# Optimization experiments

Measured on AMD Instinct MI355X. Metric: run time of the kernel, lower is better.

Reference implementation:

```python
import jax, jax.numpy as jnp
import numpy as np

N, L, E, H, D = 4, 2048, 1024, 16, 64

def setup_inputs() -> dict:
    key = jax.random.key(0)
    ks = jax.random.split(key, 8)
    s = 1.0 / np.sqrt(E)
    return {
        "Q": jax.random.normal(ks[0], (N, L, E), jnp.float32),
        "K": jax.random.normal(ks[1], (N, L, E), jnp.float32),
        "V": jax.random.normal(ks[2], (N, L, E), jnp.float32),
        "Wq": jax.random.normal(ks[3], (H * D, E), jnp.float32) * s,
        "bq": jnp.zeros((H * D,), jnp.float32),
        "Wk": jax.random.normal(ks[4], (H * D, E), jnp.float32) * s,
        "bk": jnp.zeros((H * D,), jnp.float32),
        "Wv": jax.random.normal(ks[5], (H * D, E), jnp.float32) * s,
        "bv": jnp.zeros((H * D,), jnp.float32),
        "Wo": jax.random.normal(ks[6], (E, H * D), jnp.float32) * s,
        "bo": jnp.zeros((E,), jnp.float32),
    }

def reference(Q, K, V, Wq, bq, Wk, bk, Wv, bv, Wo, bo):
    n, lq, e = Q.shape
    lk = K.shape[1]
    # projections: Linear(x) = x @ W.T + b
    q = (Q @ Wq.T + bq).reshape(n, lq, H, D)
    k = (K @ Wk.T + bk).reshape(n, lk, H, D)
    v = (V @ Wv.T + bv).reshape(n, lk, H, D)
    # scores over key dim (original broadcasts Q*K and sums over d)
    scores = jnp.einsum('nqhd,nkhd->nqkh', q, k) / jnp.sqrt(jnp.float32(D))
    attn = jax.nn.softmax(scores, axis=2)  # softmax over key axis
    out = jnp.einsum('nqkh,nkhd->nqhd', attn, v)
    out = out.reshape(n, lq, H * D)
    return (out @ Wo.T + bo).reshape(n, lq, E)
```

## Files before the change

kernel.cpp:

```cpp
#include <hip/hip_runtime.h>
#include <cstdint>
#include <cstddef>


typedef __bf16 bf16x8 __attribute__((ext_vector_type(8)));
typedef __bf16 bf16x4 __attribute__((ext_vector_type(4)));
typedef float f32x4 __attribute__((ext_vector_type(4)));

#define LOG2E_OVER_SQRTD 0.18033688011112042f

__device__ __forceinline__ unsigned short f2bf(float f) {
  unsigned int u = __builtin_bit_cast(unsigned int, f);
  u = (u + 0x7fffu + ((u >> 16) & 1u)) >> 16;
  return (unsigned short)u;
}

__device__ __forceinline__ void gl2lds16(const void* g, void* l) {
  __builtin_amdgcn_global_load_lds(
      (__attribute__((address_space(1))) unsigned int*)g,
      (__attribute__((address_space(3))) unsigned int*)l, 16, 0, 0);
}

struct CvtArgs {
  const float* src[4];
  unsigned short* dst[4];
};
__global__ __launch_bounds__(256) void cvt_multi_k(CvtArgs a) {
  const float* s = a.src[blockIdx.y];
  unsigned short* d = a.dst[blockIdx.y];
  size_t i = ((size_t)blockIdx.x * 256 + threadIdx.x) * 4;
  float4 v = *(const float4*)(s + i);
  ushort4 o;
  o.x = f2bf(v.x); o.y = f2bf(v.y); o.z = f2bf(v.z); o.w = f2bf(v.w);
  *(ushort4*)(d + i) = o;
}

struct GemmDesc {
  const unsigned short* A;
  const unsigned short* Bt;
  const float* bias;
  void* C;
  int N;
  int nbx_shift;
  float scale;
  int bias_row;
  int permc;
};
struct GemmPack3 {
  GemmDesc g[3];
};

template <bool OUT_F32>
__global__ __launch_bounds__(256, 2) void gemm_multi_k(GemmPack3 p) {
  __shared__ __attribute__((aligned(16))) unsigned short As[128 * 64];
  __shared__ __attribute__((aligned(16))) unsigned short Bs[128 * 64];
  const GemmDesc d = p.g[blockIdx.x >> 9];
  const int t = blockIdx.x & 511;
  const int bx = t & ((1 << d.nbx_shift) - 1);
  const int by = t >> d.nbx_shift;

  const int tid = threadIdx.x;
  const int lane = tid & 63, wave = tid >> 6;
  const int lr = lane & 15, lg = lane >> 4;
  const int rowBase = by * 128;
  const int colBase = bx * 128;
  const int wm = (wave & 1) * 64, wn = (wave >> 1) * 64;

  f32x4 acc[4][4] = {};

  const unsigned short* gA[4];
  const unsigned short* gB[4];
  unsigned short* lA[4];
  unsigned short* lB[4];
#pragma unroll
  for (int i = 0; i < 4; ++i) {
    int s = tid + i * 256;
    int row = s >> 3;
    int c = (s & 7) ^ (row & 7);
    gA[i] = d.A + (size_t)(rowBase + row) * 1024 + c * 8;
    gB[i] = d.Bt + (size_t)(colBase + row) * 1024 + c * 8;
    lA[i] = &As[s * 8];
    lB[i] = &Bs[s * 8];
  }

  for (int kt = 0; kt < 16; ++kt) {
    const int ko = kt * 64;
#pragma unroll
    for (int i = 0; i < 4; ++i) {
      gl2lds16(gA[i] + ko, lA[i]);
      gl2lds16(gB[i] + ko, lB[i]);
    }
    __syncthreads();

#pragma unroll
    for (int ks = 0; ks < 2; ++ks) {
      bf16x8 af[4], bfr[4];
#pragma unroll
      for (int mt = 0; mt < 4; ++mt) {
        int row = wm + mt * 16 + lr;
        int c = (ks * 4 + lg) ^ (row & 7);
        af[mt] = *(const bf16x8*)&As[row * 64 + c * 8];
      }
#pragma unroll
      for (int nt = 0; nt < 4; ++nt) {
        int row = wn + nt * 16 + lr;
        int c = (ks * 4 + lg) ^ (row & 7);
        bfr[nt] = *(const bf16x8*)&Bs[row * 64 + c * 8];
      }
#pragma unroll
      for (int mt = 0; mt < 4; ++mt)
#pragma unroll
        for (int nt = 0; nt < 4; ++nt)
          acc[mt][nt] = __builtin_amdgcn_mfma_f32_16x16x32_bf16(
              af[mt], bfr[nt], acc[mt][nt], 0, 0, 0);
    }
    __syncthreads();
  }

#pragma unroll
  for (int mt = 0; mt < 4; ++mt)
#pragma unroll
    for (int nt = 0; nt < 4; ++nt) {
      int col = colBase + wn + nt * 16 + lr;
      int colStore = d.permc ? (colBase + wn + lr * 4 + nt) : col;
      float bcol = d.bias_row ? 0.f : d.bias[col];
#pragma unroll
      for (int r = 0; r < 4; ++r) {
        int row = rowBase + wm + mt * 16 + lg * 4 + r;
        float b = d.bias_row ? d.bias[row] : bcol;
        float val = (acc[mt][nt][r] + b) * d.scale;
        size_t idx = (size_t)row * (size_t)d.N + (size_t)colStore;
        if (OUT_F32)
          ((float*)d.C)[idx] = val;
        else
          ((unsigned short*)d.C)[idx] = f2bf(val);
      }
    }
}

__global__ __launch_bounds__(256, 4) void attn_k(
    const unsigned short* __restrict__ qb,
    const unsigned short* __restrict__ kb,
    const unsigned short* __restrict__ vtb,
    unsigned short* __restrict__ aob) {
  __shared__ __attribute__((aligned(16))) unsigned short Ks[64 * 64];
  __shared__ __attribute__((aligned(16))) unsigned short Vts[64 * 64];
  __shared__ __attribute__((aligned(16))) unsigned short QPs[4 * 32 * 72];

  const int tid = threadIdx.x;
  const int lane = tid & 63, wave = tid >> 6;
  const int lr = lane & 15, lg = lane >> 4;

  const int bid = blockIdx.x;
  const int qt = bid & 15;
  const int nh = bid >> 4;
  const int h = nh & 15, n = nh >> 4;
  const int q0 = qt * 128;

#pragma unroll
  for (int i = 0; i < 4; ++i) {
    int s = i * 256 + tid;
    int row = s >> 3;
    int c = (s & 7) ^ (row & 7);
    gl2lds16(qb + (((size_t)n * 2048 + q0 + row) << 10) + h * 64 + c * 8,
             &QPs[s * 8]);
  }
#pragma unroll
  for (int i = 0; i < 2; ++i) {
    int s = i * 256 + tid;
    int row = s >> 3;
    int c = (s & 7) ^ (row & 7);
    gl2lds16(kb + (((size_t)n * 2048 + row) << 10) + h * 64 + c * 8, &Ks[s * 8]);
    gl2lds16(vtb + (((size_t)(h * 64 + row)) << 13) + (size_t)n * 2048 + c * 8,
             &Vts[s * 8]);
  }
  __syncthreads();

  bf16x8 aq[2][2];
#pragma unroll
  for (int mt = 0; mt < 2; ++mt)
#pragma unroll
    for (int ks = 0; ks < 2; ++ks) {
      int row = wave * 32 + mt * 16 + lr;
      int c = (ks * 4 + lg) ^ (row & 7);
      aq[mt][ks] = *(const bf16x8*)&QPs[row * 64 + c * 8];
    }
  __syncthreads();

  unsigned short* PsW = &QPs[wave * (32 * 72)];

  f32x4 o_acc[2][4] = {};
  float lrow[2][4] = {};

  for (int kt = 0; kt < 32; ++kt) {
    f32x4 s_acc[2][4] = {};
#pragma unroll
    for (int ks = 0; ks < 2; ++ks)
#pragma unroll
      for (int nt = 0; nt < 4; ++nt) {
        int row = nt * 16 + lr;
        int c = (ks * 4 + lg) ^ (row & 7);
        bf16x8 bk = *(const bf16x8*)&Ks[row * 64 + c * 8];
#pragma unroll
        for (int mt = 0; mt < 2; ++mt)
          s_acc[mt][nt] = __builtin_amdgcn_mfma_f32_16x16x32_bf16(
              aq[mt][ks], bk, s_acc[mt][nt], 0, 0, 0);
      }

#pragma unroll
    for (int mt = 0; mt < 2; ++mt) {
      f32x4 p[4];
#pragma unroll
      for (int nt = 0; nt < 4; ++nt)
#pragma unroll
        for (int r = 0; r < 4; ++r)
          p[nt][r] = __builtin_amdgcn_exp2f(s_acc[mt][nt][r]);
#pragma unroll
      for (int r = 0; r < 4; ++r) {
        lrow[mt][r] += (p[0][r] + p[1][r]) + (p[2][r] + p[3][r]);
        f32x4 v4 = {p[0][r], p[1][r], p[2][r], p[3][r]};
        bf16x4 pk = __builtin_convertvector(v4, bf16x4);
        int prow = mt * 16 + lg * 4 + r;
        *(bf16x4*)&PsW[prow * 72 + lr * 4] = pk;
      }
    }

#pragma unroll
    for (int ks = 0; ks < 2; ++ks) {
      bf16x8 ap[2], bv[4];
#pragma unroll
      for (int mt = 0; mt < 2; ++mt)
        ap[mt] = *(const bf16x8*)&PsW[(mt * 16 + lr) * 72 + ks * 32 + lg * 8];
#pragma unroll
      for (int nt = 0; nt < 4; ++nt) {
        int row = nt * 16 + lr;
        int c = (ks * 4 + lg) ^ (row & 7);
        bv[nt] = *(const bf16x8*)&Vts[row * 64 + c * 8];
      }
#pragma unroll
      for (int mt = 0; mt < 2; ++mt)
#pragma unroll
        for (int nt = 0; nt < 4; ++nt)
          o_acc[mt][nt] = __builtin_amdgcn_mfma_f32_16x16x32_bf16(
              ap[mt], bv[nt], o_acc[mt][nt], 0, 0, 0);
    }

    __syncthreads();
    if (kt < 31) {
      const int k0 = (kt + 1) * 64;
#pragma unroll
      for (int i = 0; i < 2; ++i) {
        int s = i * 256 + tid;
        int row = s >> 3;
        int c = (s & 7) ^ (row & 7);
        gl2lds16(kb + (((size_t)n * 2048 + k0 + row) << 10) + h * 64 + c * 8,
                 &Ks[s * 8]);
        gl2lds16(vtb + (((size_t)(h * 64 + row)) << 13) + (size_t)n * 2048 +
                     k0 + c * 8,
                 &Vts[s * 8]);
      }
    }
    __syncthreads();
  }

#pragma unroll
  for (int mt = 0; mt < 2; ++mt)
#pragma unroll
    for (int r = 0; r < 4; ++r) {
      float l = lrow[mt][r];
      l += __shfl_xor(l, 1);
      l += __shfl_xor(l, 2);
      l += __shfl_xor(l, 4);
      l += __shfl_xor(l, 8);
      float inv = 1.0f / l;
      int row_l = q0 + wave * 32 + mt * 16 + lg * 4 + r;
      size_t base = (((size_t)n * 2048 + row_l) << 10) + h * 64;
#pragma unroll
      for (int nt = 0; nt < 4; ++nt)
        aob[base + nt * 16 + lr] = f2bf(o_acc[mt][nt][r] * inv);
    }
}

extern "C" void kernel_launch(void* const* d_in, const int* in_sizes, int n_in,
                              void* d_out, int out_size, void* d_ws,
                              size_t ws_size, hipStream_t stream) {
  const float* Q = (const float*)d_in[0];
  const float* K = (const float*)d_in[1];
  const float* V = (const float*)d_in[2];
  const float* Wq = (const float*)d_in[3];
  const float* bq = (const float*)d_in[4];
  const float* Wk = (const float*)d_in[5];
  const float* bk = (const float*)d_in[6];
  const float* Wv = (const float*)d_in[7];
  const float* bv = (const float*)d_in[8];
  const float* Wo = (const float*)d_in[9];
  const float* bo = (const float*)d_in[10];

  const size_t S = (size_t)8192 * 1024;
  const size_t W = (size_t)1024 * 1024;
  unsigned short* ws = (unsigned short*)d_ws;
  unsigned short* Qbf = ws;
  unsigned short* Kbf = ws + S;
  unsigned short* Vbf = ws + 2 * S;
  unsigned short* qbuf = ws + 3 * S;
  unsigned short* kbuf = ws + 4 * S;
  unsigned short* vtbuf = ws + 5 * S;
  unsigned short* Wqb = ws + 6 * S;
  unsigned short* Wkb = Wqb + W;
  unsigned short* Wvb = Wqb + 2 * W;
  unsigned short* Wob = Wqb + 3 * W;
  unsigned short* aob = Qbf;

  CvtArgs cx;
  cx.src[0] = Q; cx.dst[0] = Qbf;
  cx.src[1] = K; cx.dst[1] = Kbf;
  cx.src[2] = V; cx.dst[2] = Vbf;
  cx.src[3] = Q; cx.dst[3] = Qbf;
  cvt_multi_k<<<dim3(8192, 3), 256, 0, stream>>>(cx);

  CvtArgs cw;
  cw.src[0] = Wq; cw.dst[0] = Wqb;
  cw.src[1] = Wk; cw.dst[1] = Wkb;
  cw.src[2] = Wv; cw.dst[2] = Wvb;
  cw.src[3] = Wo; cw.dst[3] = Wob;
  cvt_multi_k<<<dim3(1024, 4), 256, 0, stream>>>(cw);

  GemmPack3 pp;
  pp.g[0] = {Qbf, Wqb, bq, qbuf, 1024, 3, LOG2E_OVER_SQRTD, 0, 0};
  pp.g[1] = {Kbf, Wkb, bk, kbuf, 1024, 3, 1.0f, 0, 0};
  pp.g[2] = {Wvb, Vbf, bv, vtbuf, 8192, 6, 1.0f, 1, 1};
  gemm_multi_k<false><<<1536, 256, 0, stream>>>(pp);

  attn_k<<<1024, 256, 0, stream>>>(qbuf, kbuf, vtbuf, aob);

  GemmPack3 po;
  po.g[0] = {aob, Wob, bo, d_out, 1024, 3, 1.0f, 0, 0};
  po.g[1] = po.g[0];
  po.g[2] = po.g[0];
  gemm_multi_k<true><<<512, 256, 0, stream>>>(po);
}
```

Measured before the change: 346.8 us.

## Double-buffer K/V tiles and keep P in registers via permlane swaps

The attention kernel now double-buffers the K and V tiles in LDS, prefetching the next tile before computing on the current one, so each iteration has one barrier instead of two. Swapping the MFMA operands transposes the score layout, which lets the exponentiated probabilities be packed into the PV operand with permlane32/permlane16 swaps instead of a round trip through LDS. The row-sum reduction changes to match the new layout, and one flag on the V projection GEMM changes, apparently to alter the V-transpose output layout. The cost is more LDS for the two buffers and some extra cross-lane operations.

Measured after the change: 343.3 us. About the same (-1.0%).

```diff
diff --git a/kernel.cpp b/kernel.cpp
--- a/kernel.cpp
+++ b/kernel.cpp
@@ -5,7 +5,11 @@
 
 typedef __bf16 bf16x8 __attribute__((ext_vector_type(8)));
 typedef __bf16 bf16x4 __attribute__((ext_vector_type(4)));
+typedef __bf16 bf16x2 __attribute__((ext_vector_type(2)));
 typedef float f32x4 __attribute__((ext_vector_type(4)));
+typedef float f32x2 __attribute__((ext_vector_type(2)));
+typedef unsigned int uint2v __attribute__((ext_vector_type(2)));
+typedef unsigned int uint4v __attribute__((ext_vector_type(4)));
 
 #define LOG2E_OVER_SQRTD 0.18033688011112042f
 
@@ -13,6 +17,12 @@
   unsigned int u = __builtin_bit_cast(unsigned int, f);
   u = (u + 0x7fffu + ((u >> 16) & 1u)) >> 16;
   return (unsigned short)u;
+}
+
+__device__ __forceinline__ unsigned int pk2(float a, float b) {
+  f32x2 t = {a, b};
+  bf16x2 h = __builtin_convertvector(t, bf16x2);
+  return __builtin_bit_cast(unsigned int, h);
 }
 
 __device__ __forceinline__ void gl2lds16(const void* g, void* l) {
@@ -143,9 +153,8 @@
     const unsigned short* __restrict__ kb,
     const unsigned short* __restrict__ vtb,
     unsigned short* __restrict__ aob) {
-  __shared__ __attribute__((aligned(16))) unsigned short Ks[64 * 64];
-  __shared__ __attribute__((aligned(16))) unsigned short Vts[64 * 64];
-  __shared__ __attribute__((aligned(16))) unsigned short QPs[4 * 32 * 72];
+  __shared__ __attribute__((aligned(16))) unsigned short Ks[2 * 64 * 64];
+  __shared__ __attribute__((aligned(16))) unsigned short Vts[2 * 64 * 64];
 
   const int tid = threadIdx.x;
   const int lane = tid & 63, wave = tid >> 6;
@@ -163,36 +172,59 @@
     int row = s >> 3;
     int c = (s & 7) ^ (row & 7);
     gl2lds16(qb + (((size_t)n * 2048 + q0 + row) << 10) + h * 64 + c * 8,
-             &QPs[s * 8]);
-  }
+             &Ks[s * 8]);
+  }
+  __syncthreads();
+
+  bf16x8 aq[2][2];
+#pragma unroll
+  for (int mt = 0; mt < 2; ++mt)
+#pragma unroll
+    for (int ks = 0; ks < 2; ++ks) {
+      int row = wave * 32 + mt * 16 + lr;
+      int c = (ks * 4 + lg) ^ (row & 7);
+      aq[mt][ks] = *(const bf16x8*)&Ks[row * 64 + c * 8];
+    }
+  __syncthreads();
+
+  const unsigned short* kg[2];
+  const unsigned short* vg[2];
+  int ldo[2];
 #pragma unroll
   for (int i = 0; i < 2; ++i) {
     int s = i * 256 + tid;
     int row = s >> 3;
     int c = (s & 7) ^ (row & 7);
-    gl2lds16(kb + (((size_t)n * 2048 + row) << 10) + h * 64 + c * 8, &Ks[s * 8]);
-    gl2lds16(vtb + (((size_t)(h * 64 + row)) << 13) + (size_t)n * 2048 + c * 8,
-             &Vts[s * 8]);
-  }
-  __syncthreads();
-
-  bf16x8 aq[2][2];
-#pragma unroll
-  for (int mt = 0; mt < 2; ++mt)
-#pragma unroll
-    for (int ks = 0; ks < 2; ++ks) {
-      int row = wave * 32 + mt * 16 + lr;
-      int c = (ks * 4 + lg) ^ (row & 7);
-      aq[mt][ks] = *(const bf16x8*)&QPs[row * 64 + c * 8];
-    }
-  __syncthreads();
-
-  unsigned short* PsW = &QPs[wave * (32 * 72)];
+    kg[i] = kb + (((size_t)n * 2048 + row) << 10) + h * 64 + c * 8;
+    vg[i] = vtb + (((size_t)(h * 64 + row)) << 13) + (size_t)n * 2048 + c * 8;
+    ldo[i] = s * 8;
+  }
+#pragma unroll
+  for (int i = 0; i < 2; ++i) {
+    gl2lds16(kg[i], &Ks[ldo[i]]);
+    gl2lds16(vg[i], &Vts[ldo[i]]);
+    kg[i] += 64 * 1024;
+    vg[i] += 64;
+  }
 
   f32x4 o_acc[2][4] = {};
-  float lrow[2][4] = {};
+  float lsum[2] = {};
 
   for (int kt = 0; kt < 32; ++kt) {
+    const int cb = (kt & 1) * 4096;
+    const int nb = 4096 - cb;
+    __syncthreads();
+
+    if (kt < 31) {
+#pragma unroll
+      for (int i = 0; i < 2; ++i) {
+        gl2lds16(kg[i], &Ks[nb + ldo[i]]);
+        gl2lds16(vg[i], &Vts[nb + ldo[i]]);
+        kg[i] += 64 * 1024;
+        vg[i] += 64;
+      }
+    }
+
     f32x4 s_acc[2][4] = {};
 #pragma unroll
     for (int ks = 0; ks < 2; ++ks)
@@ -200,85 +232,78 @@
       for (int nt = 0; nt < 4; ++nt) {
         int row = nt * 16 + lr;
         int c = (ks * 4 + lg) ^ (row & 7);
-        bf16x8 bk = *(const bf16x8*)&Ks[row * 64 + c * 8];
+        bf16x8 kf = *(const bf16x8*)&Ks[cb + row * 64 + c * 8];
 #pragma unroll
         for (int mt = 0; mt < 2; ++mt)
           s_acc[mt][nt] = __builtin_amdgcn_mfma_f32_16x16x32_bf16(
-              aq[mt][ks], bk, s_acc[mt][nt], 0, 0, 0);
-      }
-
+              kf, aq[mt][ks], s_acc[mt][nt], 0, 0, 0);
+      }
+
+    bf16x8 ap[2][2];
 #pragma unroll
     for (int mt = 0; mt < 2; ++mt) {
-      f32x4 p[4];
-#pragma unroll
-      for (int nt = 0; nt < 4; ++nt)
-#pragma unroll
-        for (int r = 0; r < 4; ++r)
-          p[nt][r] = __builtin_amdgcn_exp2f(s_acc[mt][nt][r]);
-#pragma unroll
-      for (int r = 0; r < 4; ++r) {
-        lrow[mt][r] += (p[0][r] + p[1][r]) + (p[2][r] + p[3][r]);
-        f32x4 v4 = {p[0][r], p[1][r], p[2][r], p[3][r]};
-        bf16x4 pk = __builtin_convertvector(v4, bf16x4);
-        int prow = mt * 16 + lg * 4 + r;
-        *(bf16x4*)&PsW[prow * 72 + lr * 4] = pk;
+#pragma unroll
+      for (int ks = 0; ks < 2; ++ks) {
+        float pe[2][4];
+#pragma unroll
+        for (int half = 0; half < 2; ++half) {
+          int nt = ks * 2 + half;
+#pragma unroll
+          for (int r = 0; r < 4; ++r)
+            pe[half][r] = __builtin_amdgcn_exp2f(s_acc[mt][nt][r]);
+          lsum[mt] += (pe[half][0] + pe[half][1]) + (pe[half][2] + pe[half][3]);
+        }
+        unsigned int x00 = pk2(pe[0][0], pe[0][1]);
+        unsigned int x01 = pk2(pe[0][2], pe[0][3]);
+        unsigned int x10 = pk2(pe[1][0], pe[1][1]);
+        unsigned int x11 = pk2(pe[1][2], pe[1][3]);
+        uint2v s0 = __builtin_amdgcn_permlane32_swap(x00, x10, false, false);
+        uint2v t0 = __builtin_amdgcn_permlane16_swap(s0[0], s0[1], false, false);
+        uint2v s1 = __builtin_amdgcn_permlane32_swap(x01, x11, false, false);
+        uint2v t1 = __builtin_amdgcn_permlane16_swap(s1[0], s1[1], false, false);
+        uint4v u;
+        u[0] = t0[0];
+        u[1] = t1[0];
+        u[2] = t0[1];
+        u[3] = t1[1];
+        ap[mt][ks] = __builtin_bit_cast(bf16x8, u);
       }
     }
 
 #pragma unroll
     for (int ks = 0; ks < 2; ++ks) {
-      bf16x8 ap[2], bv[4];
-#pragma unroll
-      for (int mt = 0; mt < 2; ++mt)
-        ap[mt] = *(const bf16x8*)&PsW[(mt * 16 + lr) * 72 + ks * 32 + lg * 8];
+      bf16x8 bv[4];
 #pragma unroll
       for (int nt = 0; nt < 4; ++nt) {
         int row = nt * 16 + lr;
         int c = (ks * 4 + lg) ^ (row & 7);
-        bv[nt] = *(const bf16x8*)&Vts[row * 64 + c * 8];
+        bv[nt] = *(const bf16x8*)&Vts[cb + row * 64 + c * 8];
       }
 #pragma unroll
       for (int mt = 0; mt < 2; ++mt)
 #pragma unroll
         for (int nt = 0; nt < 4; ++nt)
           o_acc[mt][nt] = __builtin_amdgcn_mfma_f32_16x16x32_bf16(
-              ap[mt], bv[nt], o_acc[mt][nt], 0, 0, 0);
-    }
-
-    __syncthreads();
-    if (kt < 31) {
-      const int k0 = (kt + 1) * 64;
-#pragma unroll
-      for (int i = 0; i < 2; ++i) {
-        int s = i * 256 + tid;
-        int row = s >> 3;
-        int c = (s & 7) ^ (row & 7);
-        gl2lds16(kb + (((size_t)n * 2048 + k0 + row) << 10) + h * 64 + c * 8,
-                 &Ks[s * 8]);
-        gl2lds16(vtb + (((size_t)(h * 64 + row)) << 13) + (size_t)n * 2048 +
-                     k0 + c * 8,
-                 &Vts[s * 8]);
-      }
-    }
-    __syncthreads();
-  }
-
-#pragma unroll
-  for (int mt = 0; mt < 2; ++mt)
+              ap[mt][ks], bv[nt], o_acc[mt][nt], 0, 0, 0);
+    }
+  }
+
+#pragma unroll
+  for (int mt = 0; mt < 2; ++mt) {
+    float l = lsum[mt];
+    l += __shfl_xor(l, 16);
+    l += __shfl_xor(l, 32);
 #pragma unroll
     for (int r = 0; r < 4; ++r) {
-      float l = lrow[mt][r];
-      l += __shfl_xor(l, 1);
-      l += __shfl_xor(l, 2);
-      l += __shfl_xor(l, 4);
-      l += __shfl_xor(l, 8);
-      float inv = 1.0f / l;
+      float lv = __shfl(l, lg * 4 + r);
+      float inv = 1.0f / lv;
       int row_l = q0 + wave * 32 + mt * 16 + lg * 4 + r;
       size_t base = (((size_t)n * 2048 + row_l) << 10) + h * 64;
 #pragma unroll
       for (int nt = 0; nt < 4; ++nt)
         aob[base + nt * 16 + lr] = f2bf(o_acc[mt][nt][r] * inv);
     }
+  }
 }
 
 extern "C" void kernel_launch(void* const* d_in, const int* in_sizes, int n_in,
@@ -328,7 +353,7 @@
   GemmPack3 pp;
   pp.g[0] = {Qbf, Wqb, bq, qbuf, 1024, 3, LOG2E_OVER_SQRTD, 0, 0};
   pp.g[1] = {Kbf, Wkb, bk, kbuf, 1024, 3, 1.0f, 0, 0};
-  pp.g[2] = {Wvb, Vbf, bv, vtbuf, 8192, 6, 1.0f, 1, 1};
+  pp.g[2] = {Wvb, Vbf, bv, vtbuf, 8192, 6, 1.0f, 1, 0};
   gemm_multi_k<false><<<1536, 256, 0, stream>>>(pp);
 
   attn_k<<<1024, 256, 0, stream>>>(qbuf, kbuf, vtbuf, aob);
```
